# Optimization experiments

Measured on AMD Instinct MI355X. Metric: run time of the kernel, lower is better.

## Reference

```python
import jax, jax.numpy as jnp
import numpy as np

D_MODEL = 1024
HEAD = 16
D_K = D_MODEL // HEAD
NEG_INF = -1.0e9


def setup_inputs() -> dict:
    key = jax.random.key(0)
    ks = jax.random.split(key, 12)
    B, S = 2, 2048
    scale = 1.0 / np.sqrt(D_MODEL)
    inp = {
        "query": jax.random.normal(ks[0], (B, S, D_MODEL), jnp.float32),
        "key": jax.random.normal(ks[1], (B, S, D_MODEL), jnp.float32),
        "value": jax.random.normal(ks[2], (B, S, D_MODEL), jnp.float32),
        "mask": jax.random.randint(ks[3], (B, 1, 1, S), 0, 2, jnp.int32),
        "Wq": jax.random.normal(ks[4], (D_MODEL, D_MODEL), jnp.float32) * scale,
        "bq": jnp.zeros((D_MODEL,), jnp.float32),
        "Wk": jax.random.normal(ks[5], (D_MODEL, D_MODEL), jnp.float32) * scale,
        "bk": jnp.zeros((D_MODEL,), jnp.float32),
        "Wv": jax.random.normal(ks[6], (D_MODEL, D_MODEL), jnp.float32) * scale,
        "bv": jnp.zeros((D_MODEL,), jnp.float32),
        "Wo": jax.random.normal(ks[7], (D_MODEL, D_MODEL), jnp.float32) * scale,
        "bo": jnp.zeros((D_MODEL,), jnp.float32),
    }
    return inp


def reference(query, key, value, mask, Wq, bq, Wk, bk, Wv, bv, Wo, bo):
    B, S, _ = query.shape
    # QKV projections (torch nn.Linear: x @ W^T + b)
    q = query @ Wq.T + bq
    k = key @ Wk.T + bk
    v = value @ Wv.T + bv
    # [B, H, S, d_k]
    q = q.reshape(B, S, HEAD, D_K).transpose(0, 2, 1, 3)
    k = k.reshape(B, S, HEAD, D_K).transpose(0, 2, 1, 3)
    v = v.reshape(B, S, HEAD, D_K).transpose(0, 2, 1, 3)
    # scores [B, H, S, S]
    scores = jnp.einsum("bhqd,bhkd->bhqk", q, k) / jnp.sqrt(jnp.float32(D_K))
    scores = jnp.where(mask == 0, jnp.float32(NEG_INF), scores)
    attn = jax.nn.softmax(scores, axis=-1)  # dropout off (eval mode)
    ctx = jnp.einsum("bhqk,bhkd->bhqd", attn, v)
    ctx = ctx.transpose(0, 2, 1, 3).reshape(B, S, D_MODEL)
    return ctx @ Wo.T + bo
```

## Files before the change

kernel.cpp:

```cpp
#include <hip/hip_runtime.h>
#include <cstdint>
#include <cstddef>

typedef unsigned short u16;
typedef unsigned int   u32;
typedef __bf16 bf16x8 __attribute__((ext_vector_type(8)));
typedef float  f32x4  __attribute__((ext_vector_type(4)));

#define D_MODEL 1024
#define SEQ     2048
#define NTOK    4096
#define NHEAD   16
#define DK      64

__device__ __forceinline__ float fast_exp2(float x) {
  return __builtin_amdgcn_exp2f(x);
}

__device__ __forceinline__ u16 f2bf(float f) {
  u32 u = __builtin_bit_cast(u32, f);
  u += 0x7fffu + ((u >> 16) & 1u);
  return (u16)(u >> 16);
}

__device__ __forceinline__ void gload16(const u16* g, u16* l) {
  __builtin_amdgcn_global_load_lds(
      (__attribute__((address_space(1))) void*)(uintptr_t)g,
      (__attribute__((address_space(3))) void*)l,
      16, 0, 0);
}

__global__ __launch_bounds__(256) void mask_scan(const int* __restrict__ mask,
                                                 int* __restrict__ idx,
                                                 int* __restrict__ cnt) {
  const int b = blockIdx.x, t = threadIdx.x;
  const int lane = t & 63, w = t >> 6;
  __shared__ int sW[4];
  __shared__ int sTot;
  int m8[8];
  const int base = b * SEQ + t * 8;
  int tot = 0;
#pragma unroll
  for (int i = 0; i < 8; ++i) {
    m8[i] = (mask[base + i] != 0);
    tot += m8[i];
  }
  int v = tot;
#pragma unroll
  for (int d = 1; d < 64; d <<= 1) {
    int u = __shfl_up(v, d);
    if (lane >= d) v += u;
  }
  if (lane == 63) sW[w] = v;
  __syncthreads();
  if (t == 0) {
    int run = 0;
#pragma unroll
    for (int i = 0; i < 4; ++i) { int tmp = sW[i]; sW[i] = run; run += tmp; }
    sTot = run;
  }
  __syncthreads();
  int pos = v - tot + sW[w];
#pragma unroll
  for (int i = 0; i < 8; ++i)
    if (m8[i]) idx[b * SEQ + pos++] = t * 8 + i;
  const int cn = sTot;
  if (t == 0) cnt[b] = cn;
  for (int j = cn + t; j < SEQ; j += 256) idx[b * SEQ + j] = 0;
}

__global__ __launch_bounds__(256) void w_convert(
    const float* __restrict__ wq, const float* __restrict__ wk,
    const float* __restrict__ wv, const float* __restrict__ wo,
    u16* __restrict__ wb) {
  const int total = 1 << 20;
  for (int cid = blockIdx.x * blockDim.x + threadIdx.x; cid < total;
       cid += gridDim.x * blockDim.x) {
    int which = cid >> 18;
    int off = cid & ((1 << 18) - 1);
    const float* src = which == 0 ? wq : (which == 1 ? wk : (which == 2 ? wv : wo));
    u16* dst = wb + ((size_t)which << 20);
    float4 f = ((const float4*)src)[off];
    ushort4 u;
    u.x = f2bf(f.x); u.y = f2bf(f.y); u.z = f2bf(f.z); u.w = f2bf(f.w);
    ((ushort4*)dst)[off] = u;
  }
}

__global__ __launch_bounds__(256, 3) void gemm_qkv(
    const float* __restrict__ Aq, const float* __restrict__ Ak,
    const float* __restrict__ Av, const u16* __restrict__ Bw,
    const float* __restrict__ b0, const float* __restrict__ b1,
    const float* __restrict__ b2, u16* __restrict__ Cout) {
  __shared__ __align__(16) u16 smem[3 * 128 * 64];
  u16* sA = smem;

  const int t = threadIdx.x;
  const int z = blockIdx.z;
  const float* Ap = (z == 0) ? Aq : ((z == 1) ? Ak : Av);
  const u16* Bp = Bw + ((size_t)z << 20);
  const float* bias = (z == 0) ? b0 : ((z == 1) ? b1 : b2);
  const float scl = (z == 0) ? 0.18033688011f : 1.0f;

  const int m0 = blockIdx.x * 128, n0 = blockIdx.y * 128;
  const int lane = t & 63, wv = t >> 6;
  const int wm = (wv >> 1) * 64, wn = (wv & 1) * 64;
  const int c = lane & 15, qd = lane >> 4;

  const int arow = t >> 3;
  const int aoff = (((t & 7) - arow) & 7) * 8;
  const float* gaA = Ap + (size_t)(m0 + arow) * D_MODEL + aoff;
  const u16* gaB = Bp + (size_t)(n0 + arow) * D_MODEL + aoff;

  float4 pa[4][2];
#pragma unroll
  for (int j = 0; j < 4; ++j) {
    pa[j][0] = *(const float4*)(gaA + (size_t)(32 * j) * D_MODEL);
    pa[j][1] = *(const float4*)(gaA + (size_t)(32 * j) * D_MODEL + 4);
  }
#pragma unroll
  for (int j = 0; j < 4; ++j)
    gload16(gaB + (size_t)(32 * j) * D_MODEL, smem + 8192 + (t + 256 * j) * 8);

  f32x4 acc[4][4] = {};

  for (int kbi = 0; kbi < 16; ++kbi) {
    const int cur = kbi & 1;
    __syncthreads();
#pragma unroll
    for (int j = 0; j < 4; ++j) {
      u32 w[4];
#pragma unroll
      for (int h2 = 0; h2 < 2; ++h2) {
        float4 f = pa[j][h2];
        w[2 * h2] = (u32)f2bf(f.x) | ((u32)f2bf(f.y) << 16);
        w[2 * h2 + 1] = (u32)f2bf(f.z) | ((u32)f2bf(f.w) << 16);
      }
      uint4 v4 = {w[0], w[1], w[2], w[3]};
      *(uint4*)&sA[(t + 256 * j) * 8] = v4;
    }
    __syncthreads();
    if (kbi + 1 < 16) {
      const int kb2 = (kbi + 1) * 64;
      u16* sBn = smem + 8192 + (1 - cur) * 8192;
#pragma unroll
      for (int j = 0; j < 4; ++j)
        gload16(gaB + kb2 + (size_t)(32 * j) * D_MODEL, sBn + (t + 256 * j) * 8);
#pragma unroll
      for (int j = 0; j < 4; ++j) {
        pa[j][0] = *(const float4*)(gaA + kb2 + (size_t)(32 * j) * D_MODEL);
        pa[j][1] = *(const float4*)(gaA + kb2 + (size_t)(32 * j) * D_MODEL + 4);
      }
    }
    const u16* sB = smem + 8192 + cur * 8192;
#pragma unroll
    for (int s = 0; s < 2; ++s) {
      const int ao = ((s * 4 + qd + wm + c) & 7) * 8;
      const int bo = ((s * 4 + qd + wn + c) & 7) * 8;
      bf16x8 af[4], bfr[4];
#pragma unroll
      for (int i = 0; i < 4; ++i)
        af[i] = *(const bf16x8*)&sA[(wm + i * 16 + c) * 64 + ao];
#pragma unroll
      for (int j = 0; j < 4; ++j)
        bfr[j] = *(const bf16x8*)&sB[(wn + j * 16 + c) * 64 + bo];
#pragma unroll
      for (int i = 0; i < 4; ++i)
#pragma unroll
        for (int j = 0; j < 4; ++j)
          acc[i][j] = __builtin_amdgcn_mfma_f32_16x16x32_bf16(af[i], bfr[j],
                                                              acc[i][j], 0, 0, 0);
    }
  }
  __syncthreads();

  u16* sC = smem;
  if (z == 2) {
#pragma unroll
    for (int j = 0; j < 4; ++j) {
      const int col = wn + j * 16 + c;
      const float bv = bias[n0 + col];
#pragma unroll
      for (int i = 0; i < 4; ++i)
#pragma unroll
        for (int r = 0; r < 4; ++r)
          sC[col * 136 + wm + i * 16 + qd * 4 + r] = f2bf(acc[i][j][r] + bv);
    }
    __syncthreads();
    u16* VT = Cout + ((size_t)2 << 22);
    const int bb = m0 >> 11, s0 = m0 & 2047;
    const int sidx = (t & 15) * 8;
#pragma unroll
    for (int outer = 0; outer < 8; ++outer) {
      const int vrow = outer * 16 + (t >> 4);
      const int col = n0 + vrow;
      const int hh = col >> 6, dd = col & 63;
      uint4 val = *(const uint4*)&sC[vrow * 136 + sidx];
      *(uint4*)&VT[((size_t)((bb * NHEAD + hh) * DK + dd)) * SEQ + s0 + sidx] =
          val;
    }
  } else {
#pragma unroll
    for (int j = 0; j < 4; ++j) {
      const int col = wn + j * 16 + c;
      const float bv = bias[n0 + col];
#pragma unroll
      for (int i = 0; i < 4; ++i)
#pragma unroll
        for (int r = 0; r < 4; ++r)
          sC[(wm + i * 16 + qd * 4 + r) * 136 + col] =
              f2bf((acc[i][j][r] + bv) * scl);
    }
    __syncthreads();
    u16* outp = Cout + ((size_t)z << 22);
    const int cidx = (t & 15) * 8;
#pragma unroll
    for (int outer = 0; outer < 8; ++outer) {
      const int lrow = outer * 16 + (t >> 4);
      uint4 val = *(const uint4*)&sC[lrow * 136 + cidx];
      *(uint4*)&outp[(size_t)(m0 + lrow) * D_MODEL + n0 + cidx] = val;
    }
  }
}

__global__ __launch_bounds__(256) void vtc_gather(const u16* __restrict__ VT,
                                                  const int* __restrict__ idx,
                                                  const int* __restrict__ cnt,
                                                  u16* __restrict__ VTc) {
  const int row = blockIdx.x;
  const int b = row >> 10;
  const int cn = cnt[b];
  const u16* src = VT + (size_t)row * SEQ;
  u16* dst = VTc + (size_t)row * SEQ;
  const int* ib = idx + b * SEQ;
  for (int j = threadIdx.x; j < cn; j += 256) dst[j] = src[ib[j]];
}

__global__ __launch_bounds__(256) void mha_attn(
    const u16* __restrict__ QKVb, const u16* __restrict__ VTc,
    const int* __restrict__ idx, const int* __restrict__ cnt,
    u16* __restrict__ Opart, float* __restrict__ ml) {
  __shared__ __align__(16) u16 sK[64 * 72];
  __shared__ __align__(16) u16 sVt[64 * 72];
  __shared__ __align__(16) u16 sP[128 * 72];

  const int t = threadIdx.x, lane = t & 63, wq = t >> 6;
  const int c = lane & 15, qd = lane >> 4;
  const int qb = blockIdx.x, h = blockIdx.y;
  const int b = blockIdx.z & 1, ck = blockIdx.z >> 1;

  const int cn = cnt[b];
  const int nb = (cn + 63) >> 6;
  const int half = (nb + 1) >> 1;
  const int kstart = ck ? half : 0;
  const int kend = ck ? nb : half;

  const u16* Qg = QKVb;
  const u16* Kg = QKVb + ((size_t)4 << 20);
  const u16* VTch = VTc + ((size_t)((b * NHEAD + h) * DK)) * SEQ;
  const int rowbase = b * SEQ;
  const int colbase = h * DK;

  bf16x8 aq[2][2];
#pragma unroll
  for (int qt = 0; qt < 2; ++qt) {
    const u16* g = Qg +
                   (size_t)(rowbase + qb * 128 + wq * 32 + qt * 16 + c) * D_MODEL +
                   colbase + qd * 8;
    aq[qt][0] = *(const bf16x8*)g;
    aq[qt][1] = *(const bf16x8*)(g + 32);
  }

  float l[2] = {0.f, 0.f};
  f32x4 o[2][4] = {};
  const float MADD = -1.4426950e9f;
  const float MFIX = 16.0f;

  const int r0s = t >> 2, offs = (t & 3) * 16;
  const u16* gvb = VTch + (size_t)r0s * SEQ + offs;
  const int* idxb = idx + b * SEQ + r0s;

  uint4 k0, k1, v0, v1;
  int sNext2 = 0;
  if (kstart < kend) {
    const int s0i = idxb[kstart * 64];
    const u16* gk = Kg + (size_t)(rowbase + s0i) * D_MODEL + colbase + offs;
    const u16* gv = gvb + kstart * 64;
    k0 = *(const uint4*)gk;
    k1 = *(const uint4*)(gk + 8);
    v0 = *(const uint4*)gv;
    v1 = *(const uint4*)(gv + 8);
    if (kstart + 1 < kend) sNext2 = idxb[(kstart + 1) * 64];
  }

  for (int kbi = kstart; kbi < kend; ++kbi) {
    __syncthreads();
    *(uint4*)&sK[r0s * 72 + offs] = k0;
    *(uint4*)&sK[r0s * 72 + offs + 8] = k1;
    *(uint4*)&sVt[r0s * 72 + offs] = v0;
    *(uint4*)&sVt[r0s * 72 + offs + 8] = v1;
    __syncthreads();
    if (kbi + 1 < kend) {
      const u16* gk = Kg + (size_t)(rowbase + sNext2) * D_MODEL + colbase + offs;
      const u16* gv = gvb + (kbi + 1) * 64;
      k0 = *(const uint4*)gk;
      k1 = *(const uint4*)(gk + 8);
      v0 = *(const uint4*)gv;
      v1 = *(const uint4*)(gv + 8);
    }
    if (kbi + 2 < kend) sNext2 = idxb[(kbi + 2) * 64];

    const bool full = ((kbi + 1) << 6) <= cn;
    f32x4 st[2][4];
#pragma unroll
    for (int tt = 0; tt < 4; ++tt) {
      bf16x8 ak0 = *(const bf16x8*)&sK[(tt * 16 + c) * 72 + qd * 8];
      bf16x8 ak1 = *(const bf16x8*)&sK[(tt * 16 + c) * 72 + qd * 8 + 32];
      f32x4 cin;
      if (full) {
        cin = f32x4{0.f, 0.f, 0.f, 0.f};
      } else {
        const int jb = (kbi << 6) + tt * 16 + qd * 4;
        cin = f32x4{jb + 0 < cn ? 0.f : MADD, jb + 1 < cn ? 0.f : MADD,
                    jb + 2 < cn ? 0.f : MADD, jb + 3 < cn ? 0.f : MADD};
      }
#pragma unroll
      for (int qt = 0; qt < 2; ++qt) {
        f32x4 a =
            __builtin_amdgcn_mfma_f32_16x16x32_bf16(ak0, aq[qt][0], cin, 0, 0, 0);
        a = __builtin_amdgcn_mfma_f32_16x16x32_bf16(ak1, aq[qt][1], a, 0, 0, 0);
        st[qt][tt] = a;
      }
    }

#pragma unroll
    for (int qt = 0; qt < 2; ++qt) {
      float sum = 0.f;
      const int prow = (wq * 32 + qt * 16 + c) * 72;
#pragma unroll
      for (int tt = 0; tt < 4; ++tt) {
        u32 pk[2];
#pragma unroll
        for (int pr = 0; pr < 2; ++pr) {
          u32 p0 = __builtin_bit_cast(u32, fast_exp2(st[qt][tt][2 * pr] - MFIX));
          u32 p1 =
              __builtin_bit_cast(u32, fast_exp2(st[qt][tt][2 * pr + 1] - MFIX));
          u32 hi1 = p1 & 0xffff0000u;
          pk[pr] = (p0 >> 16) | hi1;
          sum += __builtin_bit_cast(float, p0 & 0xffff0000u);
          sum += __builtin_bit_cast(float, hi1);
        }
        uint2 pv2 = {pk[0], pk[1]};
        *(uint2*)&sP[prow + tt * 16 + qd * 4] = pv2;
      }
      l[qt] += sum;
    }

    bf16x8 bp[2][2];
#pragma unroll
    for (int qt = 0; qt < 2; ++qt) {
      const int prow = (wq * 32 + qt * 16 + c) * 72;
      bp[qt][0] = *(const bf16x8*)&sP[prow + qd * 8];
      bp[qt][1] = *(const bf16x8*)&sP[prow + qd * 8 + 32];
    }
#pragma unroll
    for (int dt = 0; dt < 4; ++dt) {
      bf16x8 av0 = *(const bf16x8*)&sVt[(dt * 16 + c) * 72 + qd * 8];
      bf16x8 av1 = *(const bf16x8*)&sVt[(dt * 16 + c) * 72 + qd * 8 + 32];
#pragma unroll
      for (int qt = 0; qt < 2; ++qt) {
        o[qt][dt] =
            __builtin_amdgcn_mfma_f32_16x16x32_bf16(av0, bp[qt][0], o[qt][dt], 0, 0, 0);
        o[qt][dt] =
            __builtin_amdgcn_mfma_f32_16x16x32_bf16(av1, bp[qt][1], o[qt][dt], 0, 0, 0);
      }
    }
  }

  const size_t obase =
      (size_t)ck * 4194304 + ((size_t)((b * NHEAD + h) * SEQ) + qb * 128) * 64;
  const int mlbase = ((ck * 2 + b) * NHEAD + h) * SEQ + qb * 128;
#pragma unroll
  for (int qt = 0; qt < 2; ++qt) {
    float ls = l[qt];
    ls += __shfl_xor(ls, 16);
    ls += __shfl_xor(ls, 32);
    const float inv = (ls != 0.f) ? 1.0f / ls : 0.f;
    const int q = wq * 32 + qt * 16 + c;
#pragma unroll
    for (int dt = 0; dt < 4; ++dt) {
      u32 lo = (u32)f2bf(o[qt][dt][0] * inv) |
               ((u32)f2bf(o[qt][dt][1] * inv) << 16);
      u32 hi = (u32)f2bf(o[qt][dt][2] * inv) |
               ((u32)f2bf(o[qt][dt][3] * inv) << 16);
      uint2 ov = {lo, hi};
      *(uint2*)&Opart[obase + (size_t)q * 64 + dt * 16 + qd * 4] = ov;
    }
    if (qd == 0) ml[mlbase + q] = ls;
  }
}

__global__ __launch_bounds__(256) void mha_combine(
    const u16* __restrict__ Opart, const float* __restrict__ ml,
    u16* __restrict__ ctx) {
  const int tid = blockIdx.x * 256 + threadIdx.x;
  const int row = tid >> 3, d0 = (tid & 7) * 8;
  const int b = row >> 15, h = (row >> 11) & 15, q = row & 2047;
  float l1 = ml[row];
  float l2 = ml[65536 + row];
  float inv = 1.0f / (l1 + l2);
  float w1 = l1 * inv, w2 = l2 * inv;
  const size_t o1 = (size_t)row * 64 + d0;
  uint4 pa = *(const uint4*)(Opart + o1);
  uint4 pb = *(const uint4*)(Opart + 4194304 + o1);
  u32 wa[4] = {pa.x, pa.y, pa.z, pa.w};
  u32 wb[4] = {pb.x, pb.y, pb.z, pb.w};
  u32 out[4];
#pragma unroll
  for (int j = 0; j < 4; ++j) {
    float alo = __builtin_bit_cast(float, wa[j] << 16);
    float ahi = __builtin_bit_cast(float, wa[j] & 0xffff0000u);
    float blo = __builtin_bit_cast(float, wb[j] << 16);
    float bhi = __builtin_bit_cast(float, wb[j] & 0xffff0000u);
    float rlo = w1 * alo + w2 * blo;
    float rhi = w1 * ahi + w2 * bhi;
    out[j] = (u32)f2bf(rlo) | ((u32)f2bf(rhi) << 16);
  }
  uint4 ov = {out[0], out[1], out[2], out[3]};
  *(uint4*)&ctx[((size_t)(b * SEQ + q)) * D_MODEL + h * DK + d0] = ov;
}

__global__ __launch_bounds__(256) void gemm_out(
    const u16* __restrict__ A, const u16* __restrict__ Bw,
    const float* __restrict__ bias, float* __restrict__ Cout) {
  __shared__ __align__(16) u16 sAb[2][128 * 64];
  __shared__ __align__(16) u16 sBc[2][64 * 64];

  const int t = threadIdx.x;
  const int m0 = blockIdx.x * 128, n0 = blockIdx.y * 64;
  const int lane = t & 63, wv = t >> 6;
  const int wm = (wv >> 1) * 64, wn = (wv & 1) * 32;
  const int c = lane & 15, qd = lane >> 4;

  const int arow = t >> 3;
  const int aoff = (((t & 7) - arow) & 7) * 8;
  const u16* gaA = A + (size_t)(m0 + arow) * D_MODEL + aoff;
  const u16* gaB = Bw + (size_t)(n0 + arow) * D_MODEL + aoff;

#pragma unroll
  for (int j = 0; j < 4; ++j)
    gload16(gaA + (size_t)(32 * j) * D_MODEL, &sAb[0][(t + 256 * j) * 8]);
#pragma unroll
  for (int j = 0; j < 2; ++j)
    gload16(gaB + (size_t)(32 * j) * D_MODEL, &sBc[0][(t + 256 * j) * 8]);

  f32x4 acc[4][2] = {};

  for (int kbi = 0; kbi < 16; ++kbi) {
    const int cur = kbi & 1;
    __syncthreads();
    if (kbi + 1 < 16) {
      const int kb2 = (kbi + 1) * 64;
#pragma unroll
      for (int j = 0; j < 4; ++j)
        gload16(gaA + kb2 + (size_t)(32 * j) * D_MODEL,
                &sAb[1 - cur][(t + 256 * j) * 8]);
#pragma unroll
      for (int j = 0; j < 2; ++j)
        gload16(gaB + kb2 + (size_t)(32 * j) * D_MODEL,
                &sBc[1 - cur][(t + 256 * j) * 8]);
    }
    const u16* sA = sAb[cur];
    const u16* sB = sBc[cur];
#pragma unroll
    for (int s = 0; s < 2; ++s) {
      const int ao = ((s * 4 + qd + wm + c) & 7) * 8;
      const int bo = ((s * 4 + qd + wn + c) & 7) * 8;
      bf16x8 af[4], bfr[2];
#pragma unroll
      for (int i = 0; i < 4; ++i)
        af[i] = *(const bf16x8*)&sA[(wm + i * 16 + c) * 64 + ao];
#pragma unroll
      for (int j = 0; j < 2; ++j)
        bfr[j] = *(const bf16x8*)&sB[(wn + j * 16 + c) * 64 + bo];
#pragma unroll
      for (int i = 0; i < 4; ++i)
#pragma unroll
        for (int j = 0; j < 2; ++j)
          acc[i][j] = __builtin_amdgcn_mfma_f32_16x16x32_bf16(af[i], bfr[j],
                                                              acc[i][j], 0, 0, 0);
    }
  }

#pragma unroll
  for (int j = 0; j < 2; ++j) {
    const int col = n0 + wn + j * 16 + c;
    const float bv = bias[col];
#pragma unroll
    for (int i = 0; i < 4; ++i)
#pragma unroll
      for (int r = 0; r < 4; ++r) {
        const int row = m0 + wm + i * 16 + qd * 4 + r;
        Cout[(size_t)row * D_MODEL + col] = acc[i][j][r] + bv;
      }
  }
}

extern "C" void kernel_launch(void* const* d_in, const int* in_sizes, int n_in,
                              void* d_out, int out_size, void* d_ws,
                              size_t ws_size, hipStream_t stream) {
  const float* query = (const float*)d_in[0];
  const float* key   = (const float*)d_in[1];
  const float* value = (const float*)d_in[2];
  const int*   mask  = (const int*)d_in[3];
  const float* Wq = (const float*)d_in[4];
  const float* bq = (const float*)d_in[5];
  const float* Wk = (const float*)d_in[6];
  const float* bk = (const float*)d_in[7];
  const float* Wv = (const float*)d_in[8];
  const float* bv = (const float*)d_in[9];
  const float* Wo = (const float*)d_in[10];
  const float* bo = (const float*)d_in[11];

  u16* ws  = (u16*)d_ws;
  u16* Wb  = ws + ((size_t)12 << 20);
  u16* QKV = ws + ((size_t)16 << 20);
  u16* CTX = ws + ((size_t)28 << 20);
  u16* VTc = ws;
  u16* Opart = ws + ((size_t)4 << 20);
  float* ml = (float*)(ws + ((size_t)12 << 20));
  int* idxp = (int*)(ws + ((size_t)28 << 20));
  int* cntp = idxp + 2 * SEQ;

  mask_scan<<<dim3(2), dim3(256), 0, stream>>>(mask, idxp, cntp);
  w_convert<<<dim3(1024), dim3(256), 0, stream>>>(Wq, Wk, Wv, Wo, Wb);
  gemm_qkv<<<dim3(32, 8, 3), dim3(256), 0, stream>>>(query, key, value, Wb, bq,
                                                     bk, bv, QKV);
  vtc_gather<<<dim3(2048), dim3(256), 0, stream>>>(QKV + ((size_t)8 << 20), idxp,
                                                   cntp, VTc);
  mha_attn<<<dim3(16, 16, 4), dim3(256), 0, stream>>>(QKV, VTc, idxp, cntp,
                                                      Opart, ml);
  mha_combine<<<dim3(2048), dim3(256), 0, stream>>>(Opart, ml, CTX);
  gemm_out<<<dim3(32, 16), dim3(256), 0, stream>>>(CTX, Wb + ((size_t)3 << 20),
                                                   bo, (float*)d_out);
}
```

Before: 216.8 us.

## Deepen GEMM prefetch pipelines with manual waitcnt/barrier control in QKV and output GEMMs

Restructures the QKV projection GEMM's main loop so the fp32 A tile for step k+2 is loaded into registers while step k computes. The bf16 conversion and LDS store of the next A tile now happen after the MFMA work rather than in a separate synchronized phase. The loop uses hand-written s_waitcnt vmcnt and s_barrier instead of __syncthreads, and is fully unrolled. The output GEMM similarly stops double-buffering A in LDS and instead stages A through registers with a two-deep register prefetch and a single LDS buffer. The aim is better hiding of global memory latency and fewer barriers, but the hand-counted vmcnt values are fragile and full unrolling raises register pressure.

```diff
diff --git a/kernel.cpp b/kernel.cpp
--- a/kernel.cpp
+++ b/kernel.cpp
@@ -13,6 +13,10 @@
 #define NHEAD   16
 #define DK      64
 
+#define FENCE() asm volatile("" ::: "memory")
+#define SBAR()  asm volatile("s_barrier" ::: "memory")
+#define WVL(N)  asm volatile("s_waitcnt vmcnt(" #N ") lgkmcnt(0)" ::: "memory")
+
 __device__ __forceinline__ float fast_exp2(float x) {
   return __builtin_amdgcn_exp2f(x);
 }
@@ -21,6 +25,12 @@
   u32 u = __builtin_bit_cast(u32, f);
   u += 0x7fffu + ((u >> 16) & 1u);
   return (u16)(u >> 16);
+}
+
+__device__ __forceinline__ u32 pkbf(float a, float b) {
+  u16 x = __builtin_bit_cast(u16, (__bf16)a);
+  u16 y = __builtin_bit_cast(u16, (__bf16)b);
+  return (u32)x | ((u32)y << 16);
 }
 
 __device__ __forceinline__ void gload16(const u16* g, u16* l) {
@@ -113,45 +123,53 @@
   const u16* gaB = Bp + (size_t)(n0 + arow) * D_MODEL + aoff;
 
   float4 pa[4][2];
+  u32 cv[4][4];
+
 #pragma unroll
   for (int j = 0; j < 4; ++j) {
     pa[j][0] = *(const float4*)(gaA + (size_t)(32 * j) * D_MODEL);
     pa[j][1] = *(const float4*)(gaA + (size_t)(32 * j) * D_MODEL + 4);
   }
+  FENCE();
 #pragma unroll
   for (int j = 0; j < 4; ++j)
     gload16(gaB + (size_t)(32 * j) * D_MODEL, smem + 8192 + (t + 256 * j) * 8);
+  WVL(4);
+#pragma unroll
+  for (int j = 0; j < 4; ++j) {
+    cv[j][0] = pkbf(pa[j][0].x, pa[j][0].y);
+    cv[j][1] = pkbf(pa[j][0].z, pa[j][0].w);
+    cv[j][2] = pkbf(pa[j][1].x, pa[j][1].y);
+    cv[j][3] = pkbf(pa[j][1].z, pa[j][1].w);
+  }
+  FENCE();
+#pragma unroll
+  for (int j = 0; j < 4; ++j) {
+    pa[j][0] = *(const float4*)(gaA + 64 + (size_t)(32 * j) * D_MODEL);
+    pa[j][1] = *(const float4*)(gaA + 64 + (size_t)(32 * j) * D_MODEL + 4);
+  }
+  FENCE();
+#pragma unroll
+  for (int j = 0; j < 4; ++j) {
+    uint4 v4 = {cv[j][0], cv[j][1], cv[j][2], cv[j][3]};
+    *(uint4*)&sA[(t + 256 * j) * 8] = v4;
+  }
 
   f32x4 acc[4][4] = {};
 
+#pragma unroll
   for (int kbi = 0; kbi < 16; ++kbi) {
     const int cur = kbi & 1;
-    __syncthreads();
-#pragma unroll
-    for (int j = 0; j < 4; ++j) {
-      u32 w[4];
-#pragma unroll
-      for (int h2 = 0; h2 < 2; ++h2) {
-        float4 f = pa[j][h2];
-        w[2 * h2] = (u32)f2bf(f.x) | ((u32)f2bf(f.y) << 16);
-        w[2 * h2 + 1] = (u32)f2bf(f.z) | ((u32)f2bf(f.w) << 16);
-      }
-      uint4 v4 = {w[0], w[1], w[2], w[3]};
-      *(uint4*)&sA[(t + 256 * j) * 8] = v4;
-    }
-    __syncthreads();
+    if (kbi == 15) { WVL(0); } else { WVL(8); }
+    SBAR();
     if (kbi + 1 < 16) {
+      u16* sBn = smem + 8192 + (1 - cur) * 8192;
       const int kb2 = (kbi + 1) * 64;
-      u16* sBn = smem + 8192 + (1 - cur) * 8192;
 #pragma unroll
       for (int j = 0; j < 4; ++j)
         gload16(gaB + kb2 + (size_t)(32 * j) * D_MODEL, sBn + (t + 256 * j) * 8);
-#pragma unroll
-      for (int j = 0; j < 4; ++j) {
-        pa[j][0] = *(const float4*)(gaA + kb2 + (size_t)(32 * j) * D_MODEL);
-        pa[j][1] = *(const float4*)(gaA + kb2 + (size_t)(32 * j) * D_MODEL + 4);
-      }
-    }
+    }
+    FENCE();
     const u16* sB = smem + 8192 + cur * 8192;
 #pragma unroll
     for (int s = 0; s < 2; ++s) {
@@ -170,6 +188,31 @@
         for (int j = 0; j < 4; ++j)
           acc[i][j] = __builtin_amdgcn_mfma_f32_16x16x32_bf16(af[i], bfr[j],
                                                               acc[i][j], 0, 0, 0);
+    }
+    if (kbi + 1 < 16) {
+      WVL(4);
+#pragma unroll
+      for (int j = 0; j < 4; ++j) {
+        cv[j][0] = pkbf(pa[j][0].x, pa[j][0].y);
+        cv[j][1] = pkbf(pa[j][0].z, pa[j][0].w);
+        cv[j][2] = pkbf(pa[j][1].x, pa[j][1].y);
+        cv[j][3] = pkbf(pa[j][1].z, pa[j][1].w);
+      }
+      if (kbi + 2 < 16) {
+        const int kb3 = (kbi + 2) * 64;
+#pragma unroll
+        for (int j = 0; j < 4; ++j) {
+          pa[j][0] = *(const float4*)(gaA + kb3 + (size_t)(32 * j) * D_MODEL);
+          pa[j][1] = *(const float4*)(gaA + kb3 + (size_t)(32 * j) * D_MODEL + 4);
+        }
+      }
+      FENCE();
+      SBAR();
+#pragma unroll
+      for (int j = 0; j < 4; ++j) {
+        uint4 v4 = {cv[j][0], cv[j][1], cv[j][2], cv[j][3]};
+        *(uint4*)&sA[(t + 256 * j) * 8] = v4;
+      }
     }
   }
   __syncthreads();
@@ -433,7 +476,7 @@
 __global__ __launch_bounds__(256) void gemm_out(
     const u16* __restrict__ A, const u16* __restrict__ Bw,
     const float* __restrict__ bias, float* __restrict__ Cout) {
-  __shared__ __align__(16) u16 sAb[2][128 * 64];
+  __shared__ __align__(16) u16 sA[128 * 64];
   __shared__ __align__(16) u16 sBc[2][64 * 64];
 
   const int t = threadIdx.x;
@@ -447,30 +490,38 @@
   const u16* gaA = A + (size_t)(m0 + arow) * D_MODEL + aoff;
   const u16* gaB = Bw + (size_t)(n0 + arow) * D_MODEL + aoff;
 
+  uint4 pa[2][4];
+
 #pragma unroll
   for (int j = 0; j < 4; ++j)
-    gload16(gaA + (size_t)(32 * j) * D_MODEL, &sAb[0][(t + 256 * j) * 8]);
+    pa[0][j] = *(const uint4*)(gaA + (size_t)(32 * j) * D_MODEL);
+  FENCE();
 #pragma unroll
   for (int j = 0; j < 2; ++j)
     gload16(gaB + (size_t)(32 * j) * D_MODEL, &sBc[0][(t + 256 * j) * 8]);
+  FENCE();
+#pragma unroll
+  for (int j = 0; j < 4; ++j)
+    pa[1][j] = *(const uint4*)(gaA + 64 + (size_t)(32 * j) * D_MODEL);
+  WVL(6);
+#pragma unroll
+  for (int j = 0; j < 4; ++j) *(uint4*)&sA[(t + 256 * j) * 8] = pa[0][j];
 
   f32x4 acc[4][2] = {};
 
+#pragma unroll
   for (int kbi = 0; kbi < 16; ++kbi) {
     const int cur = kbi & 1;
-    __syncthreads();
+    if (kbi == 15) { WVL(0); } else { WVL(4); }
+    SBAR();
     if (kbi + 1 < 16) {
       const int kb2 = (kbi + 1) * 64;
-#pragma unroll
-      for (int j = 0; j < 4; ++j)
-        gload16(gaA + kb2 + (size_t)(32 * j) * D_MODEL,
-                &sAb[1 - cur][(t + 256 * j) * 8]);
 #pragma unroll
       for (int j = 0; j < 2; ++j)
         gload16(gaB + kb2 + (size_t)(32 * j) * D_MODEL,
                 &sBc[1 - cur][(t + 256 * j) * 8]);
     }
-    const u16* sA = sAb[cur];
+    FENCE();
     const u16* sB = sBc[cur];
 #pragma unroll
     for (int s = 0; s < 2; ++s) {
@@ -489,6 +540,20 @@
         for (int j = 0; j < 2; ++j)
           acc[i][j] = __builtin_amdgcn_mfma_f32_16x16x32_bf16(af[i], bfr[j],
                                                               acc[i][j], 0, 0, 0);
+    }
+    if (kbi + 1 < 16) {
+      WVL(2);
+      if (kbi + 2 < 16) {
+        const int kb3 = (kbi + 2) * 64;
+#pragma unroll
+        for (int j = 0; j < 4; ++j)
+          pa[kbi & 1][j] = *(const uint4*)(gaA + kb3 + (size_t)(32 * j) * D_MODEL);
+      }
+      FENCE();
+      SBAR();
+#pragma unroll
+      for (int j = 0; j < 4; ++j)
+        *(uint4*)&sA[(t + 256 * j) * 8] = pa[(kbi + 1) & 1][j];
     }
   }
 
```

Result: slower. 250.4 us (+15.5%).
